# Optimization experiments

Hardware: AMD Instinct MI355X
Metric: run time of the kernel (lower is better)

Reference implementation:

```python
import jax, jax.numpy as jnp
import numpy as np

B, T, D, F, H = 512, 48, 128, 16, 512


def setup_inputs() -> dict:
    key = jax.random.key(0)
    ks = jax.random.split(key, 7)
    return {
        "input": jax.random.normal(ks[0], (B, T, D, F), dtype=jnp.float32),
        "attn_w": jax.random.normal(ks[1], (2 * H + F * T,), dtype=jnp.float32) * 0.02,
        "attn_b": jax.random.normal(ks[2], (1,), dtype=jnp.float32) * 0.02,
        "w_ih": jax.random.normal(ks[3], (4 * H, D * F), dtype=jnp.float32) * 0.02,
        "w_hh": jax.random.normal(ks[4], (4 * H, H), dtype=jnp.float32) * 0.02,
        "b_ih": jax.random.normal(ks[5], (4 * H,), dtype=jnp.float32) * 0.02,
        "b_hh": jax.random.normal(ks[6], (4 * H,), dtype=jnp.float32) * 0.02,
    }


def reference(input, attn_w, attn_b, w_ih, w_hh, b_ih, b_hh):
    Bsz, Ts, Dn, Fn = input.shape
    Hs = w_hh.shape[1]
    # permute(0,2,3,1): [B, T, D, F] -> [B, D, F, T]
    x_perm = jnp.transpose(input, (0, 2, 3, 1))
    x_flat = x_perm.reshape(Bsz, Dn, Fn * Ts)  # [B, D, F*T]
    # encode_attn input is concat(hidden, cell, x); split the weight accordingly
    w_h, w_c, w_x = attn_w[:Hs], attn_w[Hs:2 * Hs], attn_w[2 * Hs:]
    # x contribution to attention logits is constant across steps
    e_x = x_flat @ w_x + attn_b[0]             # [B, D]
    xs = jnp.moveaxis(x_perm, 3, 0)            # [T, B, D, F] (time-major for scan)
    bias = b_ih + b_hh                         # fuse the two LSTM biases

    def step(carry, x_t):
        h, c = carry                           # [B, H] each
        e = e_x + (h @ w_h)[:, None] + (c @ w_c)[:, None]  # [B, D]
        a = jax.nn.softmax(e, axis=-1)
        x_hat = (a[:, :, None] * x_t).reshape(Bsz, Dn * Fn)  # [B, D*F]
        gates = x_hat @ w_ih.T + h @ w_hh.T + bias            # [B, 4H]
        i, f, g, o = jnp.split(gates, 4, axis=-1)  # torch LSTM gate order
        c_new = jax.nn.sigmoid(f) * c + jax.nn.sigmoid(i) * jnp.tanh(g)
        h_new = jax.nn.sigmoid(o) * jnp.tanh(c_new)
        return (h_new, c_new), h_new

    h0 = jnp.zeros((Bsz, Hs), dtype=input.dtype)
    _, hs = jax.lax.scan(step, (h0, h0), xs)   # hs: [T, B, H]
    return jnp.transpose(hs, (1, 0, 2))        # [B, T, H] == hidden_states[:, 1:]
```

## Files before the change

kernel.cpp:

```cpp
#include <hip/hip_runtime.h>

#define B_ 512
#define T_ 48
#define D_ 128
#define F_ 16
#define H_ 512

typedef float f32x4 __attribute__((ext_vector_type(4)));
typedef short s16x8 __attribute__((ext_vector_type(8)));
typedef unsigned short u16x8 __attribute__((ext_vector_type(8)));
typedef unsigned short u16x4 __attribute__((ext_vector_type(4)));
typedef unsigned long long u64;

__device__ __forceinline__ unsigned short f2bf(float x) {
  unsigned u = __float_as_uint(x);
  u += 0x7fffu + ((u >> 16) & 1u);
  return (unsigned short)(u >> 16);
}
__device__ __forceinline__ float bf2f(unsigned short h) {
  return __uint_as_float(((unsigned)h) << 16);
}
__device__ __forceinline__ float sigmoidf_(float x) {
  return 1.f / (1.f + expf(-x));
}

__device__ __forceinline__ void st_sys_u64(u64* p, u64 v) {
  __hip_atomic_store(p, v, __ATOMIC_RELAXED, __HIP_MEMORY_SCOPE_SYSTEM);
}
__device__ __forceinline__ u64 ld_sys_u64(const u64* p) {
  return __hip_atomic_load((u64*)p, __ATOMIC_RELAXED, __HIP_MEMORY_SCOPE_SYSTEM);
}
__device__ __forceinline__ void st_sys_u32(unsigned* p, unsigned v) {
  __hip_atomic_store(p, v, __ATOMIC_RELAXED, __HIP_MEMORY_SCOPE_SYSTEM);
}
__device__ __forceinline__ unsigned ld_sys_u32(const unsigned* p) {
  return __hip_atomic_load((unsigned*)p, __ATOMIC_RELAXED, __HIP_MEMORY_SCOPE_SYSTEM);
}

#define AS1 __attribute__((address_space(1)))
#define AS3 __attribute__((address_space(3)))
__device__ __forceinline__ void g2lds16(const void* g, void* l) {
  __builtin_amdgcn_global_load_lds((const AS1 void*)g, (AS3 void*)l, 16, 0, 0);
}

__global__ __launch_bounds__(256) void k_prep(const float* __restrict__ wih,
                                              const float* __restrict__ whh,
                                              unsigned short* __restrict__ wih_b,
                                              unsigned short* __restrict__ whh_b) {
  long i4 = ((long)blockIdx.x * 256 + threadIdx.x) * 4;
  if (i4 < 4194304) {
    float4 v = *(const float4*)(wih + i4);
    u16x4 o = {f2bf(v.x), f2bf(v.y), f2bf(v.z), f2bf(v.w)};
    *(u16x4*)(wih_b + i4) = o;
  } else {
    long j = i4 - 4194304;
    if (j < 1048576) {
      float4 v = *(const float4*)(whh + j);
      u16x4 o = {f2bf(v.x), f2bf(v.y), f2bf(v.z), f2bf(v.w)};
      *(u16x4*)(whh_b + j) = o;
    }
  }
}

__global__ __launch_bounds__(128) void k_ex(const float* __restrict__ in,
                                            const float* __restrict__ attn_w,
                                            const float* __restrict__ attn_b,
                                            float* __restrict__ a_out) {
  __shared__ float wx[768];
  __shared__ float red[128];
  const int b = blockIdx.x, d = threadIdx.x;
  for (int i = d; i < 768; i += 128) wx[i] = attn_w[1024 + i];
  __syncthreads();
  const float* base = in + (long)b * 98304 + (long)d * 16;
  float acc = 0.f;
  for (int t = 0; t < 48; ++t) {
    const float4* p = (const float4*)(base + (long)t * 2048);
    float4 v0 = p[0], v1 = p[1], v2 = p[2], v3 = p[3];
    acc += v0.x * wx[t]       + v0.y * wx[48 + t]  + v0.z * wx[96 + t]  + v0.w * wx[144 + t];
    acc += v1.x * wx[192 + t] + v1.y * wx[240 + t] + v1.z * wx[288 + t] + v1.w * wx[336 + t];
    acc += v2.x * wx[384 + t] + v2.y * wx[432 + t] + v2.z * wx[480 + t] + v2.w * wx[528 + t];
    acc += v3.x * wx[576 + t] + v3.y * wx[624 + t] + v3.z * wx[672 + t] + v3.w * wx[720 + t];
  }
  acc += attn_b[0];
  red[d] = acc;
  __syncthreads();
  for (int s = 64; s > 0; s >>= 1) {
    if (d < s) red[d] = fmaxf(red[d], red[d + s]);
    __syncthreads();
  }
  float mx = red[0];
  __syncthreads();
  float ex = expf(acc - mx);
  red[d] = ex;
  __syncthreads();
  for (int s = 64; s > 0; s >>= 1) {
    if (d < s) red[d] += red[d + s];
    __syncthreads();
  }
  a_out[b * 128 + d] = ex / red[0];
}

__global__ __launch_bounds__(256) void k_xhat(const float* __restrict__ in,
                                              const float* __restrict__ a,
                                              unsigned short* __restrict__ xh) {
  const int mrow = blockIdx.x;
  const int t = mrow >> 9, b = mrow & 511;
  const int tid = threadIdx.x;
  const int k = tid * 8;
  const int d = k >> 4;
  const int f0 = k & 15;
  const float* src = in + (((long)(b * 48 + t) * 128 + d) * 16 + f0);
  float4 v0 = *(const float4*)src;
  float4 v1 = *(const float4*)(src + 4);
  float s = a[b * 128 + d];
  u16x8 o;
  o[0] = f2bf(v0.x * s); o[1] = f2bf(v0.y * s); o[2] = f2bf(v0.z * s); o[3] = f2bf(v0.w * s);
  o[4] = f2bf(v1.x * s); o[5] = f2bf(v1.y * s); o[6] = f2bf(v1.z * s); o[7] = f2bf(v1.w * s);
  *(u16x8*)(xh + (long)mrow * 2048 + k) = o;
}

__global__ __launch_bounds__(256) void k_gemm(const unsigned short* __restrict__ A,
                                              const unsigned short* __restrict__ Bw,
                                              unsigned short* __restrict__ C) {
  __shared__ unsigned short Asm[128 * 64];
  __shared__ unsigned short Bsm[128 * 64];
  const int tid = threadIdx.x;
  const int wave = tid >> 6, lane = tid & 63;
  const int q = lane >> 4, l16 = lane & 15;
  const int id = blockIdx.x;
  const int xcd = id & 7, j = id >> 3;
  const long m0 = ((long)xcd * 24 + (j >> 4)) * 128;
  const long n0 = (long)(j & 15) * 128;
  const int wm = wave & 1, wn = wave >> 1;
  f32x4 acc[4][4];
  f32x4 zz = {0.f, 0.f, 0.f, 0.f};
#pragma unroll
  for (int i = 0; i < 4; ++i)
#pragma unroll
    for (int j2 = 0; j2 < 4; ++j2) acc[i][j2] = zz;
  const int srow = wave * 32 + (lane >> 3);
  const int csw = (lane & 7) ^ (srow & 7);
  const unsigned short* Ag = A + (m0 + srow) * 2048 + csw * 8;
  const unsigned short* Bg = Bw + (n0 + srow) * 2048 + csw * 8;
  for (int kt = 0; kt < 32; ++kt) {
    __syncthreads();
#pragma unroll
    for (int i = 0; i < 4; ++i) {
      g2lds16(Ag + (long)kt * 64 + (long)i * 8 * 2048, Asm + (wave * 32 + i * 8) * 64);
      g2lds16(Bg + (long)kt * 64 + (long)i * 8 * 2048, Bsm + (wave * 32 + i * 8) * 64);
    }
    asm volatile("s_waitcnt vmcnt(0)" ::: "memory");
    __syncthreads();
#pragma unroll
    for (int ks = 0; ks < 64; ks += 32) {
      const int ca = (ks >> 3) + q;
      const int px = (ca ^ (l16 & 7)) * 8;
      s16x8 af[4], bv[4];
#pragma unroll
      for (int mt = 0; mt < 4; ++mt)
        af[mt] = *(const s16x8*)&Asm[(wm * 64 + mt * 16 + l16) * 64 + px];
#pragma unroll
      for (int nt = 0; nt < 4; ++nt)
        bv[nt] = *(const s16x8*)&Bsm[(wn * 64 + nt * 16 + l16) * 64 + px];
#pragma unroll
      for (int mt = 0; mt < 4; ++mt)
#pragma unroll
        for (int nt = 0; nt < 4; ++nt)
          acc[mt][nt] = __builtin_amdgcn_mfma_f32_16x16x32_bf16(af[mt], bv[nt], acc[mt][nt], 0, 0, 0);
    }
  }
#pragma unroll
  for (int mt = 0; mt < 4; ++mt)
#pragma unroll
    for (int nt = 0; nt < 4; ++nt)
#pragma unroll
      for (int r = 0; r < 4; ++r) {
        long m = m0 + wm * 64 + mt * 16 + q * 4 + r;
        long n = n0 + wn * 64 + nt * 16 + l16;
        C[m * 2048 + n] = f2bf(acc[mt][nt][r]);
      }
}

__global__ __launch_bounds__(256, 1) void k_rec(const unsigned short* __restrict__ gx,
                                                const unsigned short* __restrict__ whh_b,
                                                const float* __restrict__ b_ih,
                                                const float* __restrict__ b_hh,
                                                unsigned short* __restrict__ h_buf,
                                                float* __restrict__ out,
                                                unsigned int* __restrict__ bar) {
  __shared__ unsigned short hs[32 * 528];
  __shared__ float gsm[4 * 32 * 36];
  const int tid = threadIdx.x;
  const int wave = tid >> 6, lane = tid & 63;
  const int q = lane >> 4, l16 = lane & 15;
  const int bt = blockIdx.x & 15, g = blockIdx.x >> 4;
  const int b0 = bt * 32;
  const int pm = tid >> 3, pr = (tid & 7) * 4;
  const int srow = tid >> 3, st7 = tid & 7;
  unsigned int* slots = &bar[bt * 16];

  s16x8 wreg[32];
#pragma unroll
  for (int nt = 0; nt < 2; ++nt) {
    const unsigned short* wp = whh_b + (long)(wave * 512 + g * 32 + nt * 16 + l16) * 512 + q * 8;
#pragma unroll
    for (int kk = 0; kk < 16; ++kk)
      wreg[nt * 16 + kk] = *(const s16x8*)(wp + kk * 32);
  }
#pragma unroll
  for (int i = 0; i < 32; ++i) asm volatile("" : "+v"(wreg[i]));

  float bias_[16];
#pragma unroll
  for (int qq = 0; qq < 4; ++qq)
#pragma unroll
    for (int rr = 0; rr < 4; ++rr) {
      int j = qq * 512 + g * 32 + pr + rr;
      bias_[qq * 4 + rr] = b_ih[j] + b_hh[j];
    }
  float creg[4] = {0.f, 0.f, 0.f, 0.f};
  const f32x4 zz = {0.f, 0.f, 0.f, 0.f};

  for (int t = 0; t < 48; ++t) {
    u16x4 gxr[4];
    const unsigned short* gp = gx + ((long)t * 512 + b0 + pm) * 2048 + g * 32 + pr;
#pragma unroll
    for (int qq = 0; qq < 4; ++qq) gxr[qq] = *(const u16x4*)(gp + qq * 512);

    f32x4 acc[2][2] = {{zz, zz}, {zz, zz}};
    if (t > 0) {
      if (wave == 0 && lane < 16) {
        while (ld_sys_u32(&slots[lane]) < (unsigned)t)
          __builtin_amdgcn_s_sleep(1);
      }
      __syncthreads();
      const u64* hp = (const u64*)(h_buf + ((t - 1) & 1) * (512 * 512) + (long)b0 * 512);
      u64 tmp[16];
#pragma unroll
      for (int j = 0; j < 16; ++j)
        tmp[j] = ld_sys_u64(hp + (long)srow * 128 + st7 + 8 * j);
#pragma unroll
      for (int j = 0; j < 16; ++j)
        *(u64*)&hs[srow * 528 + (st7 + 8 * j) * 4] = tmp[j];
      __syncthreads();
#pragma unroll
      for (int kk = 0; kk < 16; ++kk) {
        s16x8 af0 = *(const s16x8*)&hs[l16 * 528 + kk * 32 + q * 8];
        s16x8 af1 = *(const s16x8*)&hs[(16 + l16) * 528 + kk * 32 + q * 8];
        acc[0][0] = __builtin_amdgcn_mfma_f32_16x16x32_bf16(af0, wreg[kk],      acc[0][0], 0, 0, 0);
        acc[0][1] = __builtin_amdgcn_mfma_f32_16x16x32_bf16(af0, wreg[16 + kk], acc[0][1], 0, 0, 0);
        acc[1][0] = __builtin_amdgcn_mfma_f32_16x16x32_bf16(af1, wreg[kk],      acc[1][0], 0, 0, 0);
        acc[1][1] = __builtin_amdgcn_mfma_f32_16x16x32_bf16(af1, wreg[16 + kk], acc[1][1], 0, 0, 0);
      }
    }
#pragma unroll
    for (int mt = 0; mt < 2; ++mt)
#pragma unroll
      for (int nt = 0; nt < 2; ++nt)
        *(f32x4*)&gsm[(wave * 32 + nt * 16 + l16) * 36 + mt * 16 + q * 4] = acc[mt][nt];
    __syncthreads();
    float hval[4];
#pragma unroll
    for (int rr = 0; rr < 4; ++rr) {
      float gv[4];
#pragma unroll
      for (int qq = 0; qq < 4; ++qq)
        gv[qq] = gsm[(qq * 32 + pr + rr) * 36 + pm] + bf2f(gxr[qq][rr]) + bias_[qq * 4 + rr];
      float is = sigmoidf_(gv[0]);
      float fs = sigmoidf_(gv[1]);
      float gt = tanhf(gv[2]);
      float os = sigmoidf_(gv[3]);
      creg[rr] = fs * creg[rr] + is * gt;
      hval[rr] = os * tanhf(creg[rr]);
    }
    u16x4 hb = {f2bf(hval[0]), f2bf(hval[1]), f2bf(hval[2]), f2bf(hval[3])};
    u64 hb8;
    __builtin_memcpy(&hb8, &hb, 8);
    st_sys_u64((u64*)&h_buf[(t & 1) * (512 * 512) + (b0 + pm) * 512 + g * 32 + pr], hb8);
    f32x4 ov = {hval[0], hval[1], hval[2], hval[3]};
    __builtin_nontemporal_store(ov, (f32x4*)&out[(long)(b0 + pm) * (T_ * H_) + (long)t * H_ + g * 32 + pr]);
    __syncthreads();
    if (t < 47 && tid == 0)
      st_sys_u32(&slots[g], (unsigned)(t + 1));
  }
}

extern "C" void kernel_launch(void* const* d_in, const int* in_sizes, int n_in,
                              void* d_out, int out_size, void* d_ws, size_t ws_size,
                              hipStream_t stream) {
  const float* input  = (const float*)d_in[0];
  const float* attn_w = (const float*)d_in[1];
  const float* attn_b = (const float*)d_in[2];
  const float* w_ih   = (const float*)d_in[3];
  const float* w_hh   = (const float*)d_in[4];
  const float* b_ih   = (const float*)d_in[5];
  const float* b_hh   = (const float*)d_in[6];
  float* out = (float*)d_out;

  char* ws = (char*)d_ws;
  unsigned int* bar     = (unsigned int*)ws;
  float* a_ws           = (float*)(ws + 1024);
  unsigned short* h_buf = (unsigned short*)(ws + 263168);
  unsigned short* whh_b = (unsigned short*)(ws + 1311744);
  unsigned short* wih_b = (unsigned short*)(ws + 3408896);
  unsigned short* x_hat = (unsigned short*)(ws + 11797504);
  unsigned short* gxws  = (unsigned short*)(ws + 112460800);

  (void)hipMemsetAsync(d_ws, 0, 1024, stream);
  hipLaunchKernelGGL(k_prep, dim3(5120), dim3(256), 0, stream, w_ih, w_hh, wih_b, whh_b);
  hipLaunchKernelGGL(k_ex, dim3(512), dim3(128), 0, stream, input, attn_w, attn_b, a_ws);
  hipLaunchKernelGGL(k_xhat, dim3(24576), dim3(256), 0, stream, input, a_ws, x_hat);
  hipLaunchKernelGGL(k_gemm, dim3(3072), dim3(256), 0, stream, x_hat, wih_b, gxws);
  hipLaunchKernelGGL(k_rec, dim3(256), dim3(256), 0, stream, gxws, whh_b, b_ih, b_hh, h_buf, out, bar);
}
```

Measured before the change: 772.2 us.

## Rewrite input-projection GEMM with 256x256 tiles and double-buffered LDS pipeline

The x_hat @ W_ih GEMM moves from 128x128 tiles with 256 threads and a synchronous load-then-compute loop to 256x256 tiles with 512 threads. It uses double-buffered 128KB LDS, and global-to-LDS prefetch runs ahead of MFMA work, gated by partial vmcnt waits. Explicit barriers, setprio and sched_barrier interleave the loads with the math. The aim is to hide global load latency and raise operand reuse, at the cost of heavy LDS use per block and a hand-tuned schedule that is fragile.

```diff
diff --git a/kernel.cpp b/kernel.cpp
--- a/kernel.cpp
+++ b/kernel.cpp
@@ -119,66 +119,155 @@
   *(u16x8*)(xh + (long)mrow * 2048 + k) = o;
 }
 
-__global__ __launch_bounds__(256) void k_gemm(const unsigned short* __restrict__ A,
-                                              const unsigned short* __restrict__ Bw,
-                                              unsigned short* __restrict__ C) {
-  __shared__ unsigned short Asm[128 * 64];
-  __shared__ unsigned short Bsm[128 * 64];
+
+#define G_STAGE(ktv, ksv)                                                       \
+  do {                                                                          \
+    const long ko_ = (long)(ktv) * 64 + (ksv) * 32;                             \
+    char* la_ = (char*)SM + ((ktv) & 1) * 32768 + (ksv) * 16384 + ldsw;         \
+    g2lds16(Ag + ko_, la_);                                                     \
+    g2lds16(Ag + ko_ + 262144, la_ + 8192);                                     \
+    g2lds16(Bg + ko_, la_ + 65536);                                             \
+    g2lds16(Bg + ko_ + 262144, la_ + 73728);                                    \
+  } while (0)
+
+#define G_LDA(bufel, ksv, mh)                                                   \
+  do {                                                                          \
+    const unsigned short* ab_ = SM + (bufel) + (ksv) * 8192 + aoff0 + (mh) * 2048; \
+    af[0] = *(const s16x8*)(ab_);                                               \
+    af[1] = *(const s16x8*)(ab_ + 512);                                         \
+    af[2] = *(const s16x8*)(ab_ + 1024);                                        \
+    af[3] = *(const s16x8*)(ab_ + 1536);                                        \
+  } while (0)
+
+#define G_LDB(bufel, ksv)                                                       \
+  do {                                                                          \
+    const unsigned short* bb_ = SM + (bufel) + (ksv) * 8192 + boff0;            \
+    bv[0] = *(const s16x8*)(bb_);                                               \
+    bv[1] = *(const s16x8*)(bb_ + 512);                                         \
+    bv[2] = *(const s16x8*)(bb_ + 1024);                                        \
+    bv[3] = *(const s16x8*)(bb_ + 1536);                                        \
+  } while (0)
+
+#define G_BARW()                                                                \
+  do {                                                                          \
+    __builtin_amdgcn_s_barrier();                                               \
+    asm volatile("s_waitcnt lgkmcnt(0)" ::: "memory");                          \
+    __builtin_amdgcn_sched_barrier(0);                                          \
+  } while (0)
+
+#define G_MMA(mh)                                                               \
+  do {                                                                          \
+    __builtin_amdgcn_s_setprio(1);                                              \
+    _Pragma("unroll") for (int mt_ = 0; mt_ < 4; ++mt_)                         \
+        _Pragma("unroll") for (int nt_ = 0; nt_ < 4; ++nt_)                     \
+            acc[(mh) * 4 + mt_][nt_] = __builtin_amdgcn_mfma_f32_16x16x32_bf16( \
+                af[mt_], bv[nt_], acc[(mh) * 4 + mt_][nt_], 0, 0, 0);           \
+    __builtin_amdgcn_s_setprio(0);                                              \
+  } while (0)
+
+#define G_GATE(n) asm volatile("s_waitcnt vmcnt(" #n ")" ::: "memory")
+
+__global__ __launch_bounds__(512, 2) void k_gemm(const unsigned short* __restrict__ A,
+                                                 const unsigned short* __restrict__ Bw,
+                                                 unsigned short* __restrict__ C) {
+  __shared__ __align__(16) unsigned short SM[65536];
   const int tid = threadIdx.x;
-  const int wave = tid >> 6, lane = tid & 63;
+  const int w = tid >> 6, lane = tid & 63;
   const int q = lane >> 4, l16 = lane & 15;
+  const int wm = w >> 2, wn = w & 3;
   const int id = blockIdx.x;
   const int xcd = id & 7, j = id >> 3;
-  const long m0 = ((long)xcd * 24 + (j >> 4)) * 128;
-  const long n0 = (long)(j & 15) * 128;
-  const int wm = wave & 1, wn = wave >> 1;
-  f32x4 acc[4][4];
-  f32x4 zz = {0.f, 0.f, 0.f, 0.f};
-#pragma unroll
-  for (int i = 0; i < 4; ++i)
+  const long m0 = ((long)xcd * 12 + (j >> 3)) * 256;
+  const long n0 = (long)(j & 7) * 256;
+
+  const int srow = w * 16 + (lane >> 2);
+  const int csrc = (lane & 3) ^ ((lane >> 2) & 3);
+  const unsigned short* Ag = A + (m0 + srow) * 2048 + csrc * 8;
+  const unsigned short* Bg = Bw + (n0 + srow) * 2048 + csrc * 8;
+  const int ldsw = w * 1024;
+
+  const int psw = (q ^ (l16 & 3)) * 8;
+  const int aoff0 = (wm * 128 + l16) * 32 + psw;
+  const int boff0 = 32768 + (wn * 64 + l16) * 32 + psw;
+
+  f32x4 acc[8][4];
+  const f32x4 zz = {0.f, 0.f, 0.f, 0.f};
+#pragma unroll
+  for (int i = 0; i < 8; ++i)
 #pragma unroll
     for (int j2 = 0; j2 < 4; ++j2) acc[i][j2] = zz;
-  const int srow = wave * 32 + (lane >> 3);
-  const int csw = (lane & 7) ^ (srow & 7);
-  const unsigned short* Ag = A + (m0 + srow) * 2048 + csw * 8;
-  const unsigned short* Bg = Bw + (n0 + srow) * 2048 + csw * 8;
-  for (int kt = 0; kt < 32; ++kt) {
-    __syncthreads();
-#pragma unroll
-    for (int i = 0; i < 4; ++i) {
-      g2lds16(Ag + (long)kt * 64 + (long)i * 8 * 2048, Asm + (wave * 32 + i * 8) * 64);
-      g2lds16(Bg + (long)kt * 64 + (long)i * 8 * 2048, Bsm + (wave * 32 + i * 8) * 64);
-    }
-    asm volatile("s_waitcnt vmcnt(0)" ::: "memory");
-    __syncthreads();
-#pragma unroll
-    for (int ks = 0; ks < 64; ks += 32) {
-      const int ca = (ks >> 3) + q;
-      const int px = (ca ^ (l16 & 7)) * 8;
-      s16x8 af[4], bv[4];
-#pragma unroll
-      for (int mt = 0; mt < 4; ++mt)
-        af[mt] = *(const s16x8*)&Asm[(wm * 64 + mt * 16 + l16) * 64 + px];
+  s16x8 af[4], bv[4];
+
+  G_STAGE(0, 0);
+  G_STAGE(0, 1);
+  G_STAGE(1, 0);
+  G_GATE(8);
+  __builtin_amdgcn_s_barrier();
+
+#pragma unroll 2
+  for (int kt = 0; kt < 30; ++kt) {
+    const int bufel = (kt & 1) * 16384;
+    G_LDB(bufel, 0); G_LDA(bufel, 0, 0);
+    G_STAGE(kt + 1, 1);
+    G_BARW(); G_MMA(0);
+    __builtin_amdgcn_s_barrier();
+    G_LDA(bufel, 0, 1);
+    G_BARW(); G_MMA(1);
+    G_GATE(8);
+    __builtin_amdgcn_s_barrier();
+    G_LDB(bufel, 1); G_LDA(bufel, 1, 0);
+    G_STAGE(kt + 2, 0);
+    G_BARW(); G_MMA(0);
+    __builtin_amdgcn_s_barrier();
+    G_LDA(bufel, 1, 1);
+    G_BARW(); G_MMA(1);
+    G_GATE(8);
+    __builtin_amdgcn_s_barrier();
+  }
+  {
+    G_LDB(0, 0); G_LDA(0, 0, 0);
+    G_STAGE(31, 1);
+    G_BARW(); G_MMA(0);
+    __builtin_amdgcn_s_barrier();
+    G_LDA(0, 0, 1);
+    G_BARW(); G_MMA(1);
+    G_GATE(8);
+    __builtin_amdgcn_s_barrier();
+    G_LDB(0, 1); G_LDA(0, 1, 0);
+    G_BARW(); G_MMA(0);
+    __builtin_amdgcn_s_barrier();
+    G_LDA(0, 1, 1);
+    G_BARW(); G_MMA(1);
+    G_GATE(4);
+    __builtin_amdgcn_s_barrier();
+  }
+  {
+    G_LDB(16384, 0); G_LDA(16384, 0, 0);
+    G_BARW(); G_MMA(0);
+    __builtin_amdgcn_s_barrier();
+    G_LDA(16384, 0, 1);
+    G_BARW(); G_MMA(1);
+    G_GATE(0);
+    __builtin_amdgcn_s_barrier();
+    G_LDB(16384, 1); G_LDA(16384, 1, 0);
+    G_BARW(); G_MMA(0);
+    __builtin_amdgcn_s_barrier();
+    G_LDA(16384, 1, 1);
+    G_BARW(); G_MMA(1);
+  }
+
+#pragma unroll
+  for (int mh = 0; mh < 2; ++mh)
+#pragma unroll
+    for (int mt = 0; mt < 4; ++mt)
 #pragma unroll
       for (int nt = 0; nt < 4; ++nt)
-        bv[nt] = *(const s16x8*)&Bsm[(wn * 64 + nt * 16 + l16) * 64 + px];
-#pragma unroll
-      for (int mt = 0; mt < 4; ++mt)
-#pragma unroll
-        for (int nt = 0; nt < 4; ++nt)
-          acc[mt][nt] = __builtin_amdgcn_mfma_f32_16x16x32_bf16(af[mt], bv[nt], acc[mt][nt], 0, 0, 0);
-    }
-  }
-#pragma unroll
-  for (int mt = 0; mt < 4; ++mt)
-#pragma unroll
-    for (int nt = 0; nt < 4; ++nt)
-#pragma unroll
-      for (int r = 0; r < 4; ++r) {
-        long m = m0 + wm * 64 + mt * 16 + q * 4 + r;
-        long n = n0 + wn * 64 + nt * 16 + l16;
-        C[m * 2048 + n] = f2bf(acc[mt][nt][r]);
-      }
+#pragma unroll
+        for (int r = 0; r < 4; ++r) {
+          long m = m0 + wm * 128 + mh * 64 + mt * 16 + q * 4 + r;
+          long n = n0 + wn * 64 + nt * 16 + l16;
+          C[m * 2048 + n] = f2bf(acc[mh * 4 + mt][nt][r]);
+        }
 }
 
 __global__ __launch_bounds__(256, 1) void k_rec(const unsigned short* __restrict__ gx,
@@ -310,6 +399,6 @@
   hipLaunchKernelGGL(k_prep, dim3(5120), dim3(256), 0, stream, w_ih, w_hh, wih_b, whh_b);
   hipLaunchKernelGGL(k_ex, dim3(512), dim3(128), 0, stream, input, attn_w, attn_b, a_ws);
   hipLaunchKernelGGL(k_xhat, dim3(24576), dim3(256), 0, stream, input, a_ws, x_hat);
-  hipLaunchKernelGGL(k_gemm, dim3(3072), dim3(256), 0, stream, x_hat, wih_b, gxws);
+  hipLaunchKernelGGL(k_gemm, dim3(768), dim3(512), 0, stream, x_hat, wih_b, gxws);
   hipLaunchKernelGGL(k_rec, dim3(256), dim3(256), 0, stream, gxws, whh_b, b_ih, b_hh, h_buf, out, bar);
 }
```

After: 757.8 us. No clear change (-1.9%).
